# Optimization experiments

Measured on AMD Instinct MI355X. Metric: run time of the kernel, lower is better.

The kernel has to match this reference:

```python
import jax, jax.numpy as jnp
import numpy as np

IN_C, OUT_C, K, STRIDE, PAD = 16, 32, 3, 1, 1


def setup_inputs() -> dict:
    key = jax.random.key(0)
    kx, kw = jax.random.split(key)
    x = jax.random.normal(kx, (2, IN_C, 8, 8, 32, 32), dtype=jnp.float32)
    # matches torch.randn init of nn.Parameter
    weight = jax.random.normal(kw, (OUT_C, IN_C, K, K, K, K), dtype=jnp.float32)
    bias = jnp.zeros((OUT_C,), dtype=jnp.float32)
    return {"x": x, "weight": weight, "bias": bias}


def _conv4d(x, weight):
    # 4 spatial dims; layout N C T D H W, weight O I kT kD kH kW.
    dn = jax.lax.ConvDimensionNumbers(
        lhs_spec=(0, 1, 2, 3, 4, 5),
        rhs_spec=(0, 1, 2, 3, 4, 5),
        out_spec=(0, 1, 2, 3, 4, 5),
    )
    return jax.lax.conv_general_dilated(
        x, weight,
        window_strides=(STRIDE,) * 4,
        padding=((PAD, PAD),) * 4,
        dimension_numbers=dn,
    )


def reference(x, weight, bias):
    # Same math as unfold(im2col) + matmul + bias in the torch module,
    # expressed as a single N-D convolution (implicit GEMM).
    out = _conv4d(x, weight)  # [B, out_c, oT, oD, oH, oW]
    return out + bias[None, :, None, None, None, None]
```

## Files before the change

### kernel.cpp

```cpp
#include <hip/hip_runtime.h>

#define IN_C  16
#define OUT_C 32
#define NB 2
#define TT 8
#define DD 8
#define HH 32
#define WW 32
#define TP 10
#define DP 10
#define HP 34
#define WPAD 34

#define XT_ROW_B  1088
#define XT_ELEMS  (NB*TP*DP*HP*2*WPAD*8)
#define WT_TAPS_P 84
#define WT_ELEMS  (WT_TAPS_P*2*OUT_C*8)

#define A_SLAB_B 12288

typedef __bf16 bf16x8 __attribute__((ext_vector_type(8)));
typedef float  f32x4  __attribute__((ext_vector_type(4)));
typedef float  f32x16 __attribute__((ext_vector_type(16)));

__device__ __forceinline__ unsigned short f2bf(float f) {
    unsigned int u = __builtin_bit_cast(unsigned int, f);
    u += 0x7fffu + ((u >> 16) & 1u);
    return (unsigned short)(u >> 16);
}

__device__ __forceinline__ void gload16(const void* g, void* l) {
    __builtin_amdgcn_global_load_lds(
        (const __attribute__((address_space(1))) unsigned int*)g,
        (__attribute__((address_space(3))) unsigned int*)l, 16, 0, 0);
}

__global__ __launch_bounds__(256) void prep_kernel(const float* __restrict__ x,
                                                   const float* __restrict__ wsrc,
                                                   unsigned short* __restrict__ xt,
                                                   unsigned short* __restrict__ wt) {
    int b = blockIdx.x;
    int tid = threadIdx.x;
    if (b < 4096) {
        __shared__ unsigned short ls[WW * IN_C];
        int h = b & 31, d = (b >> 5) & 7, t = (b >> 8) & 7, n = b >> 11;
        int c = tid >> 5, w = tid & 31;
        float v0 = x[((((size_t)(n * IN_C + c)     * TT + t) * DD + d) * HH + h) * WW + w];
        float v1 = x[((((size_t)(n * IN_C + c + 8) * TT + t) * DD + d) * HH + h) * WW + w];
        ls[w * 16 + c]     = f2bf(v0);
        ls[w * 16 + c + 8] = f2bf(v1);
        __syncthreads();
        if (tid < 68) {
            int blk = tid / 34, wl = tid % 34;
            unsigned char* row = (unsigned char*)xt +
                (size_t)(((n * TP + t + 1) * DP + d + 1) * HP + h + 1) * XT_ROW_B;
            f32x4 val = {0.f, 0.f, 0.f, 0.f};
            if (wl != 0 && wl != 33)
                val = *(const f32x4*)((const unsigned char*)ls + (wl - 1) * 32 + blk * 16);
            *(f32x4*)(row + tid * 16) = val;
        }
    } else if (b < 6800) {
        int j = b - 4096;
        int n, tp, dp, hp;
        if (j < 1360)      { n = j / 680;  int r = j % 680;  tp = (r / 340) * 9; int r2 = r % 340; dp = r2 / 34;       hp = r2 % 34; }
        else if (j < 2448) { int j2 = j - 1360; n = j2 / 544; int r = j2 % 544; tp = 1 + r / 68;  int r3 = r % 68;  dp = (r3 / 34) * 9; hp = r3 % 34; }
        else               { int j3 = j - 2448; n = j3 / 128; int r = j3 % 128; tp = 1 + r / 16;  int r4 = r % 16;  dp = 1 + r4 / 2;   hp = (r4 & 1) * 33; }
        if (tid < 68) {
            unsigned char* row = (unsigned char*)xt +
                (size_t)(((n * TP + tp) * DP + dp) * HP + hp) * XT_ROW_B;
            f32x4 z = {0.f, 0.f, 0.f, 0.f};
            *(f32x4*)(row + tid * 16) = z;
        }
    } else {
        int idx = (b - 6800) * 256 + tid;
        int tap = idx >> 9;
        int r = idx & 511;
        int icblk = r >> 8, oc = (r >> 3) & 31, i8 = r & 7;
        int ic = icblk * 8 + i8;
        float v = (tap < 81) ? wsrc[(oc * IN_C + ic) * 81 + tap] : 0.0f;
        wt[idx] = f2bf(v);
    }
}

__global__ __launch_bounds__(256, 2) void conv_main_kernel(const unsigned short* __restrict__ xt,
                                                           const unsigned short* __restrict__ wt,
                                                           const float* __restrict__ bias,
                                                           float* __restrict__ out) {
    __shared__ __align__(16) unsigned char As[3][A_SLAB_B];

    int bid = blockIdx.x;
    int lb  = (bid & 7) * 64 + (bid >> 3);
    int hb = lb & 3, d = (lb >> 2) & 7, t = (lb >> 5) & 7, n = lb >> 8;
    int h0 = hb * 8;
    int tid  = threadIdx.x;
    int wv   = tid >> 6;
    int lane = tid & 63;
    int l31  = lane & 31;
    int kblk = lane >> 5;

    int ab = kblk * 544 + l31 * 16;
    const unsigned char* wb = (const unsigned char*)wt + kblk * 512 + l31 * 16;

    auto asrc = [&](int p) {
        return (const unsigned char*)xt +
            (size_t)(((n * TP + t + p / 3) * DP + d + p % 3) * HP + h0) * XT_ROW_B;
    };

    {
        const unsigned char* s0 = asrc(0);
        const unsigned char* s1 = asrc(1);
#pragma unroll
        for (int i = 0; i < 3; ++i) {
            gload16(s0 + (tid + i * 256) * 16, As[0] + (tid + i * 256) * 16);
            gload16(s1 + (tid + i * 256) * 16, As[1] + (tid + i * 256) * 16);
        }
    }
    bf16x8 bf[2][9];
#pragma unroll
    for (int j = 0; j < 9; ++j)
        bf[0][j] = *(const bf16x8*)(wb + (size_t)j * 1024);
    asm volatile("s_waitcnt vmcnt(0)" ::: "memory");
    __syncthreads();

    f32x16 acc[2];
    acc[0] = {}; acc[1] = {};

#pragma unroll
    for (int p = 0; p < 9; ++p) {
        const int cur = p & 1, nxt = cur ^ 1;

        if (p < 8) {
            const unsigned char* bsrc = wb + (size_t)(p + 1) * 9 * 1024;
#pragma unroll
            for (int j = 0; j < 9; ++j)
                bf[nxt][j] = *(const bf16x8*)(bsrc + (size_t)j * 1024);
        }
        if (p < 7) {
            const unsigned char* src = asrc(p + 2);
            unsigned char* dst = As[(p + 2) % 3];
#pragma unroll
            for (int i = 0; i < 3; ++i)
                gload16(src + (tid + i * 256) * 16, dst + (tid + i * 256) * 16);
        }

        const unsigned char* A = As[p % 3];
#pragma unroll
        for (int rr = 0; rr < 4; ++rr) {
#pragma unroll
            for (int kw = 0; kw < 3; ++kw) {
                bf16x8 a = *(const bf16x8*)(A + (2 * wv + rr) * 1088 + ab + kw * 16);
#pragma unroll
                for (int kh = 0; kh < 3; ++kh) {
                    const int m = rr - kh;
                    if (m >= 0 && m < 2)
                        acc[m] = __builtin_amdgcn_mfma_f32_32x32x16_bf16(a, bf[cur][kh * 3 + kw], acc[m], 0, 0, 0);
                }
            }
        }

        asm volatile("s_waitcnt vmcnt(3)" ::: "memory");
        __syncthreads();
    }

    float bsv = bias[l31];
#pragma unroll
    for (int m = 0; m < 2; ++m) {
        int oh = h0 + 2 * wv + m;
        float* obase = out + (((((size_t)n * OUT_C + l31) * TT + t) * DD + d) * HH + oh) * WW;
#pragma unroll
        for (int q = 0; q < 4; ++q) {
            f32x4 v = { acc[m][4 * q + 0] + bsv, acc[m][4 * q + 1] + bsv,
                        acc[m][4 * q + 2] + bsv, acc[m][4 * q + 3] + bsv };
            *(f32x4*)(obase + 8 * q + 4 * kblk) = v;
        }
    }
}

extern "C" void kernel_launch(void* const* d_in, const int* in_sizes, int n_in,
                              void* d_out, int out_size, void* d_ws, size_t ws_size,
                              hipStream_t stream) {
    const float* x    = (const float*)d_in[0];
    const float* wsrc = (const float*)d_in[1];
    const float* bias = (const float*)d_in[2];
    float* out        = (float*)d_out;

    unsigned short* xt = (unsigned short*)d_ws;
    unsigned short* wt = xt + XT_ELEMS;

    prep_kernel<<<4096 + 2704 + 164, 256, 0, stream>>>(x, wsrc, xt, wt);
    conv_main_kernel<<<NB * TT * DD * 4, 256, 0, stream>>>(xt, wt, bias, out);
}
```

Baseline: 29.54 us.

## Give each wave its own double-buffered LDS slab and drop block barriers

Each wave now loads only the four input rows it needs into a private double-buffered LDS slab, instead of the block sharing a triple-buffered 10-row slab. This removes the per-tap __syncthreads, and waits are handled per wave with s_waitcnt on vmcnt. The cost is redundant global/L2 traffic, since neighbouring waves reload overlapping rows. The prefetch distance also drops from two taps ahead to one.

```diff
diff --git a/kernel.cpp b/kernel.cpp
--- a/kernel.cpp
+++ b/kernel.cpp
@@ -17,7 +17,7 @@
 #define WT_TAPS_P 84
 #define WT_ELEMS  (WT_TAPS_P*2*OUT_C*8)
 
-#define A_SLAB_B 12288
+#define W_SLAB_B 5120
 
 typedef __bf16 bf16x8 __attribute__((ext_vector_type(8)));
 typedef float  f32x4  __attribute__((ext_vector_type(4)));
@@ -86,7 +86,7 @@
                                                            const unsigned short* __restrict__ wt,
                                                            const float* __restrict__ bias,
                                                            float* __restrict__ out) {
-    __shared__ __align__(16) unsigned char As[3][A_SLAB_B];
+    __shared__ __align__(16) unsigned char As[4][2][W_SLAB_B];
 
     int bid = blockIdx.x;
     int lb  = (bid & 7) * 64 + (bid >> 3);
@@ -100,27 +100,26 @@
 
     int ab = kblk * 544 + l31 * 16;
     const unsigned char* wb = (const unsigned char*)wt + kblk * 512 + l31 * 16;
+    const int rowbase = h0 + 2 * wv;
 
     auto asrc = [&](int p) {
         return (const unsigned char*)xt +
-            (size_t)(((n * TP + t + p / 3) * DP + d + p % 3) * HP + h0) * XT_ROW_B;
+            (size_t)(((n * TP + t + p / 3) * DP + d + p % 3) * HP + rowbase) * XT_ROW_B;
     };
 
+    unsigned char* slab0 = As[wv][0];
+    unsigned char* slab1 = As[wv][1];
+
     {
-        const unsigned char* s0 = asrc(0);
-        const unsigned char* s1 = asrc(1);
+        const unsigned char* s = asrc(0);
 #pragma unroll
-        for (int i = 0; i < 3; ++i) {
-            gload16(s0 + (tid + i * 256) * 16, As[0] + (tid + i * 256) * 16);
-            gload16(s1 + (tid + i * 256) * 16, As[1] + (tid + i * 256) * 16);
-        }
+        for (int i = 0; i < 5; ++i)
+            gload16(s + (lane + i * 64) * 16, slab0 + (lane + i * 64) * 16);
     }
     bf16x8 bf[2][9];
 #pragma unroll
     for (int j = 0; j < 9; ++j)
         bf[0][j] = *(const bf16x8*)(wb + (size_t)j * 1024);
-    asm volatile("s_waitcnt vmcnt(0)" ::: "memory");
-    __syncthreads();
 
     f32x16 acc[2];
     acc[0] = {}; acc[1] = {};
@@ -130,25 +129,27 @@
         const int cur = p & 1, nxt = cur ^ 1;
 
         if (p < 8) {
-            const unsigned char* bsrc = wb + (size_t)(p + 1) * 9 * 1024;
+            const unsigned char* s = asrc(p + 1);
+            unsigned char* dstS = (p & 1) ? slab0 : slab1;
+#pragma unroll
+            for (int i = 0; i < 5; ++i)
+                gload16(s + (lane + i * 64) * 16, dstS + (lane + i * 64) * 16);
+            const unsigned char* bsrc = wb + (size_t)(p + 1) * 9216;
 #pragma unroll
             for (int j = 0; j < 9; ++j)
                 bf[nxt][j] = *(const bf16x8*)(bsrc + (size_t)j * 1024);
+            asm volatile("s_waitcnt vmcnt(14)" ::: "memory");
+        } else {
+            asm volatile("s_waitcnt vmcnt(0)" ::: "memory");
         }
-        if (p < 7) {
-            const unsigned char* src = asrc(p + 2);
-            unsigned char* dst = As[(p + 2) % 3];
-#pragma unroll
-            for (int i = 0; i < 3; ++i)
-                gload16(src + (tid + i * 256) * 16, dst + (tid + i * 256) * 16);
-        }
+        __builtin_amdgcn_sched_barrier(0);
 
-        const unsigned char* A = As[p % 3];
+        const unsigned char* A = (p & 1) ? slab1 : slab0;
 #pragma unroll
         for (int rr = 0; rr < 4; ++rr) {
 #pragma unroll
             for (int kw = 0; kw < 3; ++kw) {
-                bf16x8 a = *(const bf16x8*)(A + (2 * wv + rr) * 1088 + ab + kw * 16);
+                bf16x8 a = *(const bf16x8*)(A + rr * 1088 + ab + kw * 16);
 #pragma unroll
                 for (int kh = 0; kh < 3; ++kh) {
                     const int m = rr - kh;
@@ -157,9 +158,6 @@
                 }
             }
         }
-
-        asm volatile("s_waitcnt vmcnt(3)" ::: "memory");
-        __syncthreads();
     }
 
     float bsv = bias[l31];
```

Result: faster. 27.11 us (-8.2%).

## Stage weights in LDS and use 2 waves with 4 output rows each

Applied to the files above, without the earlier changes.

The conv kernel now copies the per-plane weight slab into a triple-buffered LDS region alongside the activation slab, using async global-to-LDS loads. Previously each wave fetched its weights straight from global memory into registers. The block shrinks from 4 waves to 2, and each wave accumulates 4 output rows instead of 2, which improves reuse of each A fragment across kh taps. The trade-off is more LDS per block and fewer waves to hide latency, which may reduce occupancy. The block count stays the same, so total parallelism is halved.

```diff
diff --git a/kernel.cpp b/kernel.cpp
--- a/kernel.cpp
+++ b/kernel.cpp
@@ -18,6 +18,7 @@
 #define WT_ELEMS  (WT_TAPS_P*2*OUT_C*8)
 
 #define A_SLAB_B 12288
+#define B_SLAB_B 10240
 
 typedef __bf16 bf16x8 __attribute__((ext_vector_type(8)));
 typedef float  f32x4  __attribute__((ext_vector_type(4)));
@@ -82,90 +83,84 @@
     }
 }
 
-__global__ __launch_bounds__(256, 2) void conv_main_kernel(const unsigned short* __restrict__ xt,
+__global__ __launch_bounds__(128, 1) void conv_main_kernel(const unsigned short* __restrict__ xt,
                                                            const unsigned short* __restrict__ wt,
                                                            const float* __restrict__ bias,
                                                            float* __restrict__ out) {
     __shared__ __align__(16) unsigned char As[3][A_SLAB_B];
+    __shared__ __align__(16) unsigned char Bs[3][B_SLAB_B];
 
     int bid = blockIdx.x;
     int lb  = (bid & 7) * 64 + (bid >> 3);
     int hb = lb & 3, d = (lb >> 2) & 7, t = (lb >> 5) & 7, n = lb >> 8;
     int h0 = hb * 8;
     int tid  = threadIdx.x;
-    int wv   = tid >> 6;
+    int wm   = tid >> 6;
     int lane = tid & 63;
     int l31  = lane & 31;
     int kblk = lane >> 5;
 
     int ab = kblk * 544 + l31 * 16;
-    const unsigned char* wb = (const unsigned char*)wt + kblk * 512 + l31 * 16;
+    int bb = kblk * 512 + l31 * 16;
 
-    auto asrc = [&](int p) {
-        return (const unsigned char*)xt +
+    auto issueP = [&](int p) {
+        const unsigned char* srcA = (const unsigned char*)xt +
             (size_t)(((n * TP + t + p / 3) * DP + d + p % 3) * HP + h0) * XT_ROW_B;
+        unsigned char* dstA = As[p % 3];
+#pragma unroll
+        for (int i = 0; i < 6; ++i)
+            gload16(srcA + (tid + i * 128) * 16, dstA + (tid + i * 128) * 16);
+        const unsigned char* srcB = (const unsigned char*)wt + (size_t)p * 9 * 1024;
+        unsigned char* dstB = Bs[p % 3];
+#pragma unroll
+        for (int i = 0; i < 5; ++i)
+            gload16(srcB + (tid + i * 128) * 16, dstB + (tid + i * 128) * 16);
     };
 
-    {
-        const unsigned char* s0 = asrc(0);
-        const unsigned char* s1 = asrc(1);
-#pragma unroll
-        for (int i = 0; i < 3; ++i) {
-            gload16(s0 + (tid + i * 256) * 16, As[0] + (tid + i * 256) * 16);
-            gload16(s1 + (tid + i * 256) * 16, As[1] + (tid + i * 256) * 16);
-        }
-    }
-    bf16x8 bf[2][9];
-#pragma unroll
-    for (int j = 0; j < 9; ++j)
-        bf[0][j] = *(const bf16x8*)(wb + (size_t)j * 1024);
-    asm volatile("s_waitcnt vmcnt(0)" ::: "memory");
+    issueP(0);
+    issueP(1);
+    asm volatile("s_waitcnt vmcnt(11)" ::: "memory");
     __syncthreads();
 
-    f32x16 acc[2];
-    acc[0] = {}; acc[1] = {};
+    f32x16 acc[4];
+#pragma unroll
+    for (int m = 0; m < 4; ++m) acc[m] = {};
 
 #pragma unroll
     for (int p = 0; p < 9; ++p) {
-        const int cur = p & 1, nxt = cur ^ 1;
+        if (p + 2 <= 8) issueP(p + 2);
 
-        if (p < 8) {
-            const unsigned char* bsrc = wb + (size_t)(p + 1) * 9 * 1024;
+        const unsigned char* Ab = As[p % 3];
+        const unsigned char* Bb = Bs[p % 3];
+        bf16x8 bf[9];
 #pragma unroll
-            for (int j = 0; j < 9; ++j)
-                bf[nxt][j] = *(const bf16x8*)(bsrc + (size_t)j * 1024);
-        }
-        if (p < 7) {
-            const unsigned char* src = asrc(p + 2);
-            unsigned char* dst = As[(p + 2) % 3];
+        for (int j = 0; j < 9; ++j)
+            bf[j] = *(const bf16x8*)(Bb + j * 1024 + bb);
 #pragma unroll
-            for (int i = 0; i < 3; ++i)
-                gload16(src + (tid + i * 256) * 16, dst + (tid + i * 256) * 16);
-        }
-
-        const unsigned char* A = As[p % 3];
+        for (int kw = 0; kw < 3; ++kw) {
 #pragma unroll
-        for (int rr = 0; rr < 4; ++rr) {
-#pragma unroll
-            for (int kw = 0; kw < 3; ++kw) {
-                bf16x8 a = *(const bf16x8*)(A + (2 * wv + rr) * 1088 + ab + kw * 16);
+            for (int r = 0; r < 6; ++r) {
+                bf16x8 a = *(const bf16x8*)(Ab + (4 * wm + r) * 1088 + ab + kw * 16);
 #pragma unroll
                 for (int kh = 0; kh < 3; ++kh) {
-                    const int m = rr - kh;
-                    if (m >= 0 && m < 2)
-                        acc[m] = __builtin_amdgcn_mfma_f32_32x32x16_bf16(a, bf[cur][kh * 3 + kw], acc[m], 0, 0, 0);
+                    const int m = r - kh;
+                    if (m >= 0 && m < 4)
+                        acc[m] = __builtin_amdgcn_mfma_f32_32x32x16_bf16(a, bf[kh * 3 + kw], acc[m], 0, 0, 0);
                 }
             }
         }
 
-        asm volatile("s_waitcnt vmcnt(3)" ::: "memory");
+        if (p + 2 <= 8)
+            asm volatile("s_waitcnt vmcnt(11)" ::: "memory");
+        else
+            asm volatile("s_waitcnt vmcnt(0)" ::: "memory");
         __syncthreads();
     }
 
     float bsv = bias[l31];
 #pragma unroll
-    for (int m = 0; m < 2; ++m) {
-        int oh = h0 + 2 * wv + m;
+    for (int m = 0; m < 4; ++m) {
+        int oh = h0 + 4 * wm + m;
         float* obase = out + (((((size_t)n * OUT_C + l31) * TT + t) * DD + d) * HH + oh) * WW;
 #pragma unroll
         for (int q = 0; q < 4; ++q) {
@@ -188,5 +183,5 @@
     unsigned short* wt = xt + XT_ELEMS;
 
     prep_kernel<<<4096 + 2704 + 164, 256, 0, stream>>>(x, wsrc, xt, wt);
-    conv_main_kernel<<<NB * TT * DD * 4, 256, 0, stream>>>(xt, wt, bias, out);
+    conv_main_kernel<<<NB * TT * DD * 4, 128, 0, stream>>>(xt, wt, bias, out);
 }
```

Measured after the change: 28.66 us. -3.0%, faster.

## Stage weight taps through LDS alongside activations with async global-to-LDS loads

Applied to the files above, without the earlier changes.

Weights for each (kt,kd) plane are now loaded into a triple-buffered LDS slab with global_load_lds, alongside the activation slab, instead of being read per lane into a double-buffered register array. The per-plane weight fragments are then read from LDS before the MFMA loop, and s_setprio raises wave priority around the MFMA section. This is meant to cut register pressure and let the weight and activation prefetches share one vmcnt-tracked pipeline. The cost is doubled LDS use (72KB per block), which may limit occupancy, plus extra LDS reads for the weights.

```diff
diff --git a/kernel.cpp b/kernel.cpp
--- a/kernel.cpp
+++ b/kernel.cpp
@@ -17,7 +17,7 @@
 #define WT_TAPS_P 84
 #define WT_ELEMS  (WT_TAPS_P*2*OUT_C*8)
 
-#define A_SLAB_B 12288
+#define SLAB_B 12288
 
 typedef __bf16 bf16x8 __attribute__((ext_vector_type(8)));
 typedef float  f32x4  __attribute__((ext_vector_type(4)));
@@ -86,7 +86,8 @@
                                                            const unsigned short* __restrict__ wt,
                                                            const float* __restrict__ bias,
                                                            float* __restrict__ out) {
-    __shared__ __align__(16) unsigned char As[3][A_SLAB_B];
+    __shared__ __align__(16) unsigned char As[3][SLAB_B];
+    __shared__ __align__(16) unsigned char Bs[3][SLAB_B];
 
     int bid = blockIdx.x;
     int lb  = (bid & 7) * 64 + (bid >> 3);
@@ -99,27 +100,25 @@
     int kblk = lane >> 5;
 
     int ab = kblk * 544 + l31 * 16;
-    const unsigned char* wb = (const unsigned char*)wt + kblk * 512 + l31 * 16;
+    int bb = kblk * 512 + l31 * 16;
 
-    auto asrc = [&](int p) {
-        return (const unsigned char*)xt +
+    auto issueP = [&](int p) {
+        const unsigned char* srcA = (const unsigned char*)xt +
             (size_t)(((n * TP + t + p / 3) * DP + d + p % 3) * HP + h0) * XT_ROW_B;
+        unsigned char* dstA = As[p % 3];
+#pragma unroll
+        for (int i = 0; i < 3; ++i)
+            gload16(srcA + (tid + i * 256) * 16, dstA + (tid + i * 256) * 16);
+        const unsigned char* srcB = (const unsigned char*)wt + (size_t)p * 9216;
+        unsigned char* dstB = Bs[p % 3];
+#pragma unroll
+        for (int i = 0; i < 3; ++i)
+            gload16(srcB + (tid + i * 256) * 16, dstB + (tid + i * 256) * 16);
     };
 
-    {
-        const unsigned char* s0 = asrc(0);
-        const unsigned char* s1 = asrc(1);
-#pragma unroll
-        for (int i = 0; i < 3; ++i) {
-            gload16(s0 + (tid + i * 256) * 16, As[0] + (tid + i * 256) * 16);
-            gload16(s1 + (tid + i * 256) * 16, As[1] + (tid + i * 256) * 16);
-        }
-    }
-    bf16x8 bf[2][9];
-#pragma unroll
-    for (int j = 0; j < 9; ++j)
-        bf[0][j] = *(const bf16x8*)(wb + (size_t)j * 1024);
-    asm volatile("s_waitcnt vmcnt(0)" ::: "memory");
+    issueP(0);
+    issueP(1);
+    asm volatile("s_waitcnt vmcnt(6)" ::: "memory");
     __syncthreads();
 
     f32x16 acc[2];
@@ -127,23 +126,19 @@
 
 #pragma unroll
     for (int p = 0; p < 9; ++p) {
-        const int cur = p & 1, nxt = cur ^ 1;
-
-        if (p < 8) {
-            const unsigned char* bsrc = wb + (size_t)(p + 1) * 9 * 1024;
-#pragma unroll
-            for (int j = 0; j < 9; ++j)
-                bf[nxt][j] = *(const bf16x8*)(bsrc + (size_t)j * 1024);
-        }
-        if (p < 7) {
-            const unsigned char* src = asrc(p + 2);
-            unsigned char* dst = As[(p + 2) % 3];
-#pragma unroll
-            for (int i = 0; i < 3; ++i)
-                gload16(src + (tid + i * 256) * 16, dst + (tid + i * 256) * 16);
-        }
+        if (p < 7) issueP(p + 2);
 
         const unsigned char* A = As[p % 3];
+        const unsigned char* B = Bs[p % 3];
+
+        __builtin_amdgcn_s_setprio(1);
+        bf16x8 bf[3][3];
+#pragma unroll
+        for (int kh = 0; kh < 3; ++kh)
+#pragma unroll
+            for (int kw = 0; kw < 3; ++kw)
+                bf[kh][kw] = *(const bf16x8*)(B + ((kh * 3 + kw) << 10) + bb);
+
 #pragma unroll
         for (int rr = 0; rr < 4; ++rr) {
 #pragma unroll
@@ -153,12 +148,16 @@
                 for (int kh = 0; kh < 3; ++kh) {
                     const int m = rr - kh;
                     if (m >= 0 && m < 2)
-                        acc[m] = __builtin_amdgcn_mfma_f32_32x32x16_bf16(a, bf[cur][kh * 3 + kw], acc[m], 0, 0, 0);
+                        acc[m] = __builtin_amdgcn_mfma_f32_32x32x16_bf16(a, bf[kh][kw], acc[m], 0, 0, 0);
                 }
             }
         }
+        __builtin_amdgcn_s_setprio(0);
 
-        asm volatile("s_waitcnt vmcnt(3)" ::: "memory");
+        if (p < 7)
+            asm volatile("s_waitcnt vmcnt(6)" ::: "memory");
+        else
+            asm volatile("s_waitcnt vmcnt(0)" ::: "memory");
         __syncthreads();
     }
 
```

After: 28.43 us. -3.8%, faster.
